# Kernel tuning notes

Hardware: AMD Instinct MI355X
Metric: run time of the kernel (lower is better)

## Reference

```python
import jax, jax.numpy as jnp
import numpy as np

N = 50000
E = 600000
H = 128   # hidden_channels (input to decoder)
O = 128   # output_channels (LSTM hidden size)
S = 8     # seq_len


def setup_inputs() -> dict:
    key = jax.random.key(0)
    ks = jax.random.split(key, 10)
    x = jax.random.normal(ks[0], (N, H), dtype=jnp.float32)
    c = jax.random.normal(ks[1], (N, H), dtype=jnp.float32)
    edge_index = jax.random.randint(ks[2], (2, E), 0, N, dtype=jnp.int64)
    # GCNConv weights (PyG: out = norm_agg(x @ W) + b)
    sc = lambda fan_in: 1.0 / np.sqrt(fan_in)
    Wh = jax.random.uniform(ks[3], (H, O), jnp.float32, -sc(H), sc(H))
    bh = jnp.zeros((O,), jnp.float32)
    Wc = jax.random.uniform(ks[4], (H, O), jnp.float32, -sc(H), sc(H))
    bc = jnp.zeros((O,), jnp.float32)
    # per-timestep cell convs: GCNConv(H + O, 4*O)
    Wcell = jax.random.uniform(ks[5], (S, H + O, 4 * O), jnp.float32, -sc(H + O), sc(H + O))
    bcell = jnp.zeros((S, 4 * O), jnp.float32)
    return {"x": x, "c": c, "edge_index": edge_index,
            "Wh": Wh, "bh": bh, "Wc": Wc, "bc": bc,
            "Wcell": Wcell, "bcell": bcell}


def _gcn(feat, W, b, src, dst, dinv):
    # PyG GCNConv with default add_self_loops=True, edge_weight=None:
    # out = D^{-1/2}(A+I)D^{-1/2} (feat @ W) + b
    xw = feat @ W                                   # [N, C_out]
    norm = (dinv[src] * dinv[dst])[:, None]         # [E, 1]
    agg = jax.ops.segment_sum(xw[src] * norm, dst, num_segments=N)
    agg = agg + (dinv * dinv)[:, None] * xw         # self-loop term
    return agg + b


def reference(x, c, edge_index, Wh, bh, Wc, bc, Wcell, bcell):
    src = edge_index[0]
    dst = edge_index[1]
    # degree (with self-loops, unit edge weights); computed on target index
    deg = jax.ops.segment_sum(jnp.ones((E,), jnp.float32), dst, num_segments=N) + 1.0
    dinv = 1.0 / jnp.sqrt(deg)

    h_cur = _gcn(x, Wh, bh, src, dst, dinv)
    c_cur = _gcn(c, Wc, bc, src, dst, dinv)

    def step(carry, params):
        h, cs = carry
        W, b = params
        combined = jnp.concatenate([x, h], axis=1)          # [N, H+O]
        cc = _gcn(combined, W, b, src, dst, dinv)           # [N, 4O]
        cc_f, cc_i, cc_o, cc_g = jnp.split(cc, 4, axis=1)
        f = jax.nn.sigmoid(cc_f)
        i = jax.nn.sigmoid(cc_i)
        o = jax.nn.sigmoid(cc_o)
        g = jnp.tanh(cc_g)
        c_next = f * cs + i * g
        h_next = o * jnp.tanh(c_next)
        return (h_next, c_next), h_next

    (h_fin, c_fin), hs = jax.lax.scan(step, (h_cur, c_cur), (Wcell, bcell))
    return hs, (h_fin, c_fin)  # hs: [S, N, O]
```

## Files before the change

### kernel.cpp

```cpp
#include <hip/hip_runtime.h>
#include <hip/hip_bf16.h>
#include <hip/hip_fp16.h>
#include <cstddef>


#define TPB 256

typedef __attribute__((ext_vector_type(8))) short bf16x8;
typedef __attribute__((ext_vector_type(4))) float f32x4;

__device__ __forceinline__ float sigf(float x) {
    return 1.0f / (1.0f + __expf(-x));
}
__device__ __forceinline__ float tanhfast(float x) {
    return 1.0f - 2.0f / (__expf(2.0f * x) + 1.0f);
}


__global__ void k_hist(const int* __restrict__ dst, int* __restrict__ counts, int E) {
    int e = blockIdx.x * TPB + threadIdx.x;
    if (e < E) atomicAdd(&counts[dst[e]], 1);
}

__global__ void k_scan_block(const int* __restrict__ counts, int* __restrict__ offsets,
                             int* __restrict__ sums, int N) {
    __shared__ int s[TPB];
    int tid = threadIdx.x;
    int gid = blockIdx.x * TPB + tid;
    int v = (gid < N) ? counts[gid] : 0;
    s[tid] = v;
    __syncthreads();
    for (int d = 1; d < TPB; d <<= 1) {
        int t = (tid >= d) ? s[tid - d] : 0;
        __syncthreads();
        s[tid] += t;
        __syncthreads();
    }
    if (gid < N) offsets[gid] = s[tid] - v;
    if (tid == TPB - 1) sums[blockIdx.x] = s[tid];
}

__global__ void k_scan_tops(int* __restrict__ sums, int nb) {
    __shared__ int s[TPB];
    int tid = threadIdx.x;
    int v = (tid < nb) ? sums[tid] : 0;
    s[tid] = v;
    __syncthreads();
    for (int d = 1; d < TPB; d <<= 1) {
        int t = (tid >= d) ? s[tid - d] : 0;
        __syncthreads();
        s[tid] += t;
        __syncthreads();
    }
    if (tid < nb) sums[tid] = s[tid] - v;
}

__global__ void k_scan_finish(const int* __restrict__ counts, int* __restrict__ offsets,
                              const int* __restrict__ sums, int* __restrict__ cursor,
                              float* __restrict__ dinv, int N, int E) {
    int gid = blockIdx.x * TPB + threadIdx.x;
    if (gid < N) {
        int off = offsets[gid] + sums[blockIdx.x];
        offsets[gid] = off;
        cursor[gid]  = off;
        dinv[gid]    = rsqrtf((float)(counts[gid] + 1));
    }
    if (gid == 0) offsets[N] = E;
}

__global__ void k_csr_scatter(const int* __restrict__ src, const int* __restrict__ dst,
                              const float* __restrict__ dinv, int* __restrict__ cursor,
                              int* __restrict__ csr_src, float* __restrict__ csr_w, int E) {
    int e = blockIdx.x * TPB + threadIdx.x;
    if (e >= E) return;
    int d = dst[e], s = src[e];
    int pos = atomicAdd(&cursor[d], 1);
    csr_src[pos] = s;
    csr_w[pos] = dinv[s] * dinv[d];
}


__global__ void k_f32tof16(const float* __restrict__ in, __half* __restrict__ out, int n4) {
    int i = blockIdx.x * TPB + threadIdx.x;
    if (i >= n4) return;
    float4 v = ((const float4*)in)[i];
    __half2 lo = __floats2half2_rn(v.x, v.y);
    __half2 hi = __floats2half2_rn(v.z, v.w);
    ((__half2*)out)[2 * i]     = lo;
    ((__half2*)out)[2 * i + 1] = hi;
}


__global__ __launch_bounds__(TPB) void k_aggregate_h(
        const __half* __restrict__ feat, __hip_bfloat16* __restrict__ agg,
        const int* __restrict__ offsets, const int* __restrict__ csr_src,
        const float* __restrict__ csr_w, const float* __restrict__ dinv, int N) {
    int node = blockIdx.x * 4 + (threadIdx.x >> 6);
    if (node >= N) return;
    int lane = threadIdx.x & 63;
    const __half2* f2 = (const __half2*)feat;
    float2 self = __half22float2(f2[(size_t)node * 64 + lane]);
    float di = dinv[node];
    float w0 = di * di;
    float accx = w0 * self.x, accy = w0 * self.y;
    int b = offsets[node], e = offsets[node + 1];
    int k = b;
    for (; k + 1 < e; k += 2) {
        int s0 = csr_src[k], s1 = csr_src[k + 1];
        float wa = csr_w[k], wb = csr_w[k + 1];
        float2 v0 = __half22float2(f2[(size_t)s0 * 64 + lane]);
        float2 v1 = __half22float2(f2[(size_t)s1 * 64 + lane]);
        accx = fmaf(wa, v0.x, accx);
        accy = fmaf(wa, v0.y, accy);
        accx = fmaf(wb, v1.x, accx);
        accy = fmaf(wb, v1.y, accy);
    }
    if (k < e) {
        int s = csr_src[k];
        float w = csr_w[k];
        float2 v = __half22float2(f2[(size_t)s * 64 + lane]);
        accx = fmaf(w, v.x, accx);
        accy = fmaf(w, v.y, accy);
    }
    __hip_bfloat162 r;
    r.x = __float2bfloat16(accx);
    r.y = __float2bfloat16(accy);
    ((__hip_bfloat162*)agg)[(size_t)node * 64 + lane] = r;
}

__global__ __launch_bounds__(TPB) void k_aggregate_h2(
        const __half* __restrict__ fa, const __half* __restrict__ fb,
        __hip_bfloat16* __restrict__ aggA, __hip_bfloat16* __restrict__ aggB,
        const int* __restrict__ offsets, const int* __restrict__ csr_src,
        const float* __restrict__ csr_w, const float* __restrict__ dinv, int N) {
    int node = blockIdx.x * 4 + (threadIdx.x >> 6);
    if (node >= N) return;
    int lane = threadIdx.x & 63;
    const __half2* fa2 = (const __half2*)fa;
    const __half2* fb2 = (const __half2*)fb;
    size_t selfIdx = (size_t)node * 64 + lane;
    float di = dinv[node];
    float w0 = di * di;
    float2 sa = __half22float2(fa2[selfIdx]);
    float2 sb = __half22float2(fb2[selfIdx]);
    float ax = w0 * sa.x, ay = w0 * sa.y;
    float bx = w0 * sb.x, by = w0 * sb.y;
    int b = offsets[node], e = offsets[node + 1];
    for (int k = b; k < e; ++k) {
        int s = csr_src[k];
        float w = csr_w[k];
        size_t si = (size_t)s * 64 + lane;
        float2 va = __half22float2(fa2[si]);
        float2 vb = __half22float2(fb2[si]);
        ax = fmaf(w, va.x, ax);
        ay = fmaf(w, va.y, ay);
        bx = fmaf(w, vb.x, bx);
        by = fmaf(w, vb.y, by);
    }
    __hip_bfloat162 ra, rb;
    ra.x = __float2bfloat16(ax); ra.y = __float2bfloat16(ay);
    rb.x = __float2bfloat16(bx); rb.y = __float2bfloat16(by);
    ((__hip_bfloat162*)aggA)[selfIdx] = ra;
    ((__hip_bfloat162*)aggB)[selfIdx] = rb;
}


__global__ void k_pack_w128(const float* __restrict__ W, __hip_bfloat16* __restrict__ Wp) {
    int idx = blockIdx.x * TPB + threadIdx.x;
    if (idx >= 16384) return;
    int j = idx & 7, lane = (idx >> 3) & 63, pblk = (idx >> 9) & 7, ks = idx >> 12;
    int k = ks * 32 + (lane >> 4) * 8 + j;
    int col = pblk * 16 + (lane & 15);
    Wp[idx] = __float2bfloat16(W[k * 128 + col]);
}

__global__ void k_pack_wcell(const float* __restrict__ W, __hip_bfloat16* __restrict__ Wp, int S) {
    int idx = blockIdx.x * TPB + threadIdx.x;
    if (idx >= S * 131072) return;
    int j = idx & 7, lane = (idx >> 3) & 63, pblk = (idx >> 9) & 31;
    int ks = (idx >> 14) & 7, s = idx >> 17;
    int p = pblk * 16 + (lane & 15);
    int jcol = p >> 2, gate = p & 3;
    int k = ks * 32 + (lane >> 4) * 8 + j;
    Wp[idx] = __float2bfloat16(W[(size_t)s * 131072 + k * 512 + gate * 128 + jcol]);
}


__global__ __launch_bounds__(TPB) void k_gemm_t(
        const __hip_bfloat16* __restrict__ Ap,
        const __hip_bfloat16* __restrict__ featb,
        const float* __restrict__ bias, float* __restrict__ Cout,
        __half* __restrict__ outh, int N) {
    __shared__ __align__(16) short Bs[128 * 40];
    int tid = threadIdx.x;
    int wave = tid >> 6, lane = tid & 63;
    int w_p = wave >> 1, w_n = wave & 1;
    int n0 = blockIdx.x * 128;
    int quad = lane >> 4, m16 = lane & 15;
    f32x4 zero = {0.f, 0.f, 0.f, 0.f};
    f32x4 acc[4][4];
    #pragma unroll
    for (int t = 0; t < 4; ++t)
        #pragma unroll
        for (int g = 0; g < 4; ++g) acc[t][g] = zero;

    for (int ks = 0; ks < 4; ++ks) {
        int kbase = ks * 32;
        __syncthreads();
        #pragma unroll
        for (int it = 0; it < 2; ++it) {
            int lin = it * TPB + tid;
            int row = lin >> 2, seg = lin & 3;
            int node = n0 + row;
            f32x4 v = zero;
            if (node < N) v = *(const f32x4*)(featb + (size_t)node * 128 + kbase + seg * 8);
            *(f32x4*)&Bs[row * 40 + seg * 8] = v;
        }
        __syncthreads();
        bf16x8 a[4], b[4];
        #pragma unroll
        for (int t = 0; t < 4; ++t)
            a[t] = *(const bf16x8*)(Ap + (((size_t)ks * 8 + w_p * 4 + t) * 64 + lane) * 8);
        #pragma unroll
        for (int g = 0; g < 4; ++g)
            b[g] = *(const bf16x8*)&Bs[(w_n * 64 + g * 16 + m16) * 40 + quad * 8];
        #pragma unroll
        for (int t = 0; t < 4; ++t)
            #pragma unroll
            for (int g = 0; g < 4; ++g)
                acc[t][g] = __builtin_amdgcn_mfma_f32_16x16x32_bf16(a[t], b[g], acc[t][g], 0, 0, 0);
    }
    #pragma unroll
    for (int t = 0; t < 4; ++t) {
        int p = w_p * 64 + t * 16 + quad * 4;
        f32x4 bv = *(const f32x4*)(bias + p);
        #pragma unroll
        for (int g = 0; g < 4; ++g) {
            int nd = n0 + w_n * 64 + g * 16 + m16;
            if (nd < N) {
                f32x4 o = acc[t][g] + bv;
                if (Cout) *(f32x4*)(Cout + (size_t)nd * 128 + p) = o;
                if (outh) {
                    __half2 lo = __floats2half2_rn(o.x, o.y);
                    __half2 hi = __floats2half2_rn(o.z, o.w);
                    __half2* hp = (__half2*)(outh + (size_t)nd * 128 + p);
                    hp[0] = lo;
                    hp[1] = hi;
                }
            }
        }
    }
}


__global__ __launch_bounds__(TPB) void k_cell_t(
        const __hip_bfloat16* __restrict__ Ap,
        const __hip_bfloat16* __restrict__ axb, const __hip_bfloat16* __restrict__ ahb,
        const float* __restrict__ bias,
        float* __restrict__ cbuf, float* __restrict__ hout,
        __half* __restrict__ houth,
        float* __restrict__ hfin, int N) {
    __shared__ __align__(16) short Bs[128 * 40];
    int tid = threadIdx.x;
    int wave = tid >> 6, lane = tid & 63;
    int w_p = wave >> 1, w_n = wave & 1;
    int n0 = blockIdx.x * 128;
    int p0 = blockIdx.y * 128;
    int quad = lane >> 4, m16 = lane & 15;
    f32x4 zero = {0.f, 0.f, 0.f, 0.f};
    f32x4 acc[4][4];
    #pragma unroll
    for (int t = 0; t < 4; ++t)
        #pragma unroll
        for (int g = 0; g < 4; ++g) acc[t][g] = zero;

    for (int ks = 0; ks < 8; ++ks) {
        const __hip_bfloat16* fsrc = (ks < 4) ? axb : ahb;
        int kbase = (ks & 3) * 32;
        __syncthreads();
        #pragma unroll
        for (int it = 0; it < 2; ++it) {
            int lin = it * TPB + tid;
            int row = lin >> 2, seg = lin & 3;
            int node = n0 + row;
            f32x4 v = zero;
            if (node < N) v = *(const f32x4*)(fsrc + (size_t)node * 128 + kbase + seg * 8);
            *(f32x4*)&Bs[row * 40 + seg * 8] = v;
        }
        __syncthreads();
        bf16x8 a[4], b[4];
        #pragma unroll
        for (int t = 0; t < 4; ++t)
            a[t] = *(const bf16x8*)(Ap + (((size_t)ks * 32 + (p0 >> 4) + w_p * 4 + t) * 64 + lane) * 8);
        #pragma unroll
        for (int g = 0; g < 4; ++g)
            b[g] = *(const bf16x8*)&Bs[(w_n * 64 + g * 16 + m16) * 40 + quad * 8];
        #pragma unroll
        for (int t = 0; t < 4; ++t)
            #pragma unroll
            for (int g = 0; g < 4; ++g)
                acc[t][g] = __builtin_amdgcn_mfma_f32_16x16x32_bf16(a[t], b[g], acc[t][g], 0, 0, 0);
    }
    #pragma unroll
    for (int t = 0; t < 4; ++t) {
        int p = p0 + w_p * 64 + t * 16 + quad * 4;
        int jcol = p >> 2;
        float bf = bias[jcol], bi = bias[128 + jcol], bo = bias[256 + jcol], bg = bias[384 + jcol];
        #pragma unroll
        for (int g = 0; g < 4; ++g) {
            int nd = n0 + w_n * 64 + g * 16 + m16;
            if (nd < N) {
                float fv = sigf(acc[t][g].x + bf);
                float iv = sigf(acc[t][g].y + bi);
                float ov = sigf(acc[t][g].z + bo);
                float gv = tanhfast(acc[t][g].w + bg);
                size_t idx = (size_t)nd * 128 + jcol;
                float cp = cbuf[idx];
                float cn = fmaf(fv, cp, iv * gv);
                cbuf[idx] = cn;
                float hn = ov * tanhfast(cn);
                hout[idx] = hn;
                houth[idx] = __float2half(hn);
                if (hfin) hfin[idx] = hn;
            }
        }
    }
}


extern "C" void kernel_launch(void* const* d_in, const int* in_sizes, int n_in,
                              void* d_out, int out_size, void* d_ws, size_t ws_size,
                              hipStream_t stream) {
    const float* x  = (const float*)d_in[0];
    const float* c  = (const float*)d_in[1];
    const int*   ei = (const int*)d_in[2];
    const float* Wh = (const float*)d_in[3];
    const float* bh = (const float*)d_in[4];
    const float* Wc = (const float*)d_in[5];
    const float* bc = (const float*)d_in[6];
    const float* Wcell = (const float*)d_in[7];
    const float* bcell = (const float*)d_in[8];
    float* out = (float*)d_out;

    const int N = in_sizes[0] / 128;
    const int E = in_sizes[2] / 2;
    const int S = in_sizes[7] / (256 * 512);
    const int* srcp = ei;
    const int* dstp = ei + E;

    float* hs   = out;
    float* hfin = out + (size_t)S * N * 128;
    float* cbuf = hfin + (size_t)N * 128;

    char* w = (char*)d_ws;
    size_t off = 0;
    auto alloc = [&](size_t bytes) -> void* {
        void* p = w + off;
        off += (bytes + 255) & ~(size_t)255;
        return p;
    };
    int*   counts  = (int*)alloc((size_t)N * 4);
    int*   offsets = (int*)alloc((size_t)(N + 1) * 4);
    int*   cursor  = (int*)alloc((size_t)N * 4);
    int*   sums    = (int*)alloc(256 * 4);
    int*   csr_src = (int*)alloc((size_t)E * 4);
    float* csr_w   = (float*)alloc((size_t)E * 4);
    float* dinv    = (float*)alloc((size_t)N * 4);
    __hip_bfloat16* axb = (__hip_bfloat16*)alloc((size_t)N * 128 * 2);
    __hip_bfloat16* acb = (__hip_bfloat16*)alloc((size_t)N * 128 * 2);
    __half* xh = (__half*)alloc((size_t)N * 128 * 2);
    __half* ch = (__half*)alloc((size_t)N * 128 * 2);
    __half* hh = (__half*)alloc((size_t)N * 128 * 2);
    __hip_bfloat16* WhP = (__hip_bfloat16*)alloc(16384 * 2);
    __hip_bfloat16* WcP = (__hip_bfloat16*)alloc(16384 * 2);
    __hip_bfloat16* WcellP = (__hip_bfloat16*)alloc((size_t)S * 131072 * 2);
    (void)ws_size; (void)n_in; (void)out_size;

    hipMemsetAsync(counts, 0, (size_t)N * 4, stream);
    int eblk = (E + TPB - 1) / TPB;
    int nb   = (N + TPB - 1) / TPB;
    k_hist<<<eblk, TPB, 0, stream>>>(dstp, counts, E);
    k_scan_block<<<nb, TPB, 0, stream>>>(counts, offsets, sums, N);
    k_scan_tops<<<1, TPB, 0, stream>>>(sums, nb);
    k_scan_finish<<<nb, TPB, 0, stream>>>(counts, offsets, sums, cursor, dinv, N, E);
    k_csr_scatter<<<eblk, TPB, 0, stream>>>(srcp, dstp, dinv, cursor, csr_src, csr_w, E);

    k_pack_w128<<<64, TPB, 0, stream>>>(Wh, WhP);
    k_pack_w128<<<64, TPB, 0, stream>>>(Wc, WcP);
    k_pack_wcell<<<(S * 131072 + TPB - 1) / TPB, TPB, 0, stream>>>(Wcell, WcellP, S);

    int n4 = N * 128 / 4;
    int cb = (n4 + TPB - 1) / TPB;
    k_f32tof16<<<cb, TPB, 0, stream>>>(x, xh, n4);
    k_f32tof16<<<cb, TPB, 0, stream>>>(c, ch, n4);

    int nagg = (N + 3) / 4;
    int ngt  = (N + 127) / 128;
    k_aggregate_h2<<<nagg, TPB, 0, stream>>>(xh, ch, axb, acb, offsets, csr_src, csr_w, dinv, N);
    k_gemm_t<<<ngt, TPB, 0, stream>>>(WhP, axb, bh, nullptr, hh, N);
    k_gemm_t<<<ngt, TPB, 0, stream>>>(WcP, acb, bc, cbuf, nullptr, N);

    for (int s = 0; s < S; ++s) {
        k_aggregate_h<<<nagg, TPB, 0, stream>>>(hh, acb, offsets, csr_src, csr_w, dinv, N);
        k_cell_t<<<dim3(ngt, 4), TPB, 0, stream>>>(
            WcellP + (size_t)s * 131072, axb, acb, bcell + (size_t)s * 512,
            cbuf, hs + (size_t)s * N * 128, hh, (s == S - 1) ? hfin : nullptr, N);
    }
}
```

Before: 1.518 ms.

## Interleave CSR src/weight, unroll aggregation, and stage full node tile once in cell GEMM

The CSR source index and edge weight now sit together in one int2 array, so each edge needs a single 8-byte load instead of two separate loads. The aggregation loops are unrolled further to keep more gathers in flight. The cell kernel now stages the whole 128-node by 256-K feature tile in LDS once and loops over all four gate-column blocks inside one block. This removes the 4x re-read of features across blockIdx.y and the per-k-step barriers. In exchange it uses about 80KB of LDS per block and launches a quarter as many blocks, which lowers occupancy and parallelism.

```diff
diff --git a/kernel.cpp b/kernel.cpp
--- a/kernel.cpp
+++ b/kernel.cpp
@@ -70,13 +70,15 @@
 
 __global__ void k_csr_scatter(const int* __restrict__ src, const int* __restrict__ dst,
                               const float* __restrict__ dinv, int* __restrict__ cursor,
-                              int* __restrict__ csr_src, float* __restrict__ csr_w, int E) {
+                              int2* __restrict__ csr_sw, int E) {
     int e = blockIdx.x * TPB + threadIdx.x;
     if (e >= E) return;
     int d = dst[e], s = src[e];
     int pos = atomicAdd(&cursor[d], 1);
-    csr_src[pos] = s;
-    csr_w[pos] = dinv[s] * dinv[d];
+    int2 r;
+    r.x = s;
+    r.y = __float_as_int(dinv[s] * dinv[d]);
+    csr_sw[pos] = r;
 }
 
 
@@ -93,8 +95,8 @@
 
 __global__ __launch_bounds__(TPB) void k_aggregate_h(
         const __half* __restrict__ feat, __hip_bfloat16* __restrict__ agg,
-        const int* __restrict__ offsets, const int* __restrict__ csr_src,
-        const float* __restrict__ csr_w, const float* __restrict__ dinv, int N) {
+        const int* __restrict__ offsets, const int2* __restrict__ sw,
+        const float* __restrict__ dinv, int N) {
     int node = blockIdx.x * 4 + (threadIdx.x >> 6);
     if (node >= N) return;
     int lane = threadIdx.x & 63;
@@ -105,20 +107,23 @@
     float accx = w0 * self.x, accy = w0 * self.y;
     int b = offsets[node], e = offsets[node + 1];
     int k = b;
-    for (; k + 1 < e; k += 2) {
-        int s0 = csr_src[k], s1 = csr_src[k + 1];
-        float wa = csr_w[k], wb = csr_w[k + 1];
-        float2 v0 = __half22float2(f2[(size_t)s0 * 64 + lane]);
-        float2 v1 = __half22float2(f2[(size_t)s1 * 64 + lane]);
-        accx = fmaf(wa, v0.x, accx);
-        accy = fmaf(wa, v0.y, accy);
-        accx = fmaf(wb, v1.x, accx);
-        accy = fmaf(wb, v1.y, accy);
-    }
-    if (k < e) {
-        int s = csr_src[k];
-        float w = csr_w[k];
-        float2 v = __half22float2(f2[(size_t)s * 64 + lane]);
+    for (; k + 3 < e; k += 4) {
+        int2 e0 = sw[k], e1 = sw[k + 1], e2 = sw[k + 2], e3 = sw[k + 3];
+        float2 v0 = __half22float2(f2[(size_t)e0.x * 64 + lane]);
+        float2 v1 = __half22float2(f2[(size_t)e1.x * 64 + lane]);
+        float2 v2 = __half22float2(f2[(size_t)e2.x * 64 + lane]);
+        float2 v3 = __half22float2(f2[(size_t)e3.x * 64 + lane]);
+        float wa = __int_as_float(e0.y), wb = __int_as_float(e1.y);
+        float wc = __int_as_float(e2.y), wd = __int_as_float(e3.y);
+        accx = fmaf(wa, v0.x, accx); accy = fmaf(wa, v0.y, accy);
+        accx = fmaf(wb, v1.x, accx); accy = fmaf(wb, v1.y, accy);
+        accx = fmaf(wc, v2.x, accx); accy = fmaf(wc, v2.y, accy);
+        accx = fmaf(wd, v3.x, accx); accy = fmaf(wd, v3.y, accy);
+    }
+    for (; k < e; ++k) {
+        int2 e0 = sw[k];
+        float2 v = __half22float2(f2[(size_t)e0.x * 64 + lane]);
+        float w = __int_as_float(e0.y);
         accx = fmaf(w, v.x, accx);
         accy = fmaf(w, v.y, accy);
     }
@@ -131,8 +136,8 @@
 __global__ __launch_bounds__(TPB) void k_aggregate_h2(
         const __half* __restrict__ fa, const __half* __restrict__ fb,
         __hip_bfloat16* __restrict__ aggA, __hip_bfloat16* __restrict__ aggB,
-        const int* __restrict__ offsets, const int* __restrict__ csr_src,
-        const float* __restrict__ csr_w, const float* __restrict__ dinv, int N) {
+        const int* __restrict__ offsets, const int2* __restrict__ sw,
+        const float* __restrict__ dinv, int N) {
     int node = blockIdx.x * 4 + (threadIdx.x >> 6);
     if (node >= N) return;
     int lane = threadIdx.x & 63;
@@ -146,16 +151,29 @@
     float ax = w0 * sa.x, ay = w0 * sa.y;
     float bx = w0 * sb.x, by = w0 * sb.y;
     int b = offsets[node], e = offsets[node + 1];
-    for (int k = b; k < e; ++k) {
-        int s = csr_src[k];
-        float w = csr_w[k];
-        size_t si = (size_t)s * 64 + lane;
-        float2 va = __half22float2(fa2[si]);
-        float2 vb = __half22float2(fb2[si]);
-        ax = fmaf(w, va.x, ax);
-        ay = fmaf(w, va.y, ay);
-        bx = fmaf(w, vb.x, bx);
-        by = fmaf(w, vb.y, by);
+    int k = b;
+    for (; k + 1 < e; k += 2) {
+        int2 e0 = sw[k], e1 = sw[k + 1];
+        size_t i0 = (size_t)e0.x * 64 + lane;
+        size_t i1 = (size_t)e1.x * 64 + lane;
+        float2 va0 = __half22float2(fa2[i0]);
+        float2 vb0 = __half22float2(fb2[i0]);
+        float2 va1 = __half22float2(fa2[i1]);
+        float2 vb1 = __half22float2(fb2[i1]);
+        float wa = __int_as_float(e0.y), wb = __int_as_float(e1.y);
+        ax = fmaf(wa, va0.x, ax); ay = fmaf(wa, va0.y, ay);
+        bx = fmaf(wa, vb0.x, bx); by = fmaf(wa, vb0.y, by);
+        ax = fmaf(wb, va1.x, ax); ay = fmaf(wb, va1.y, ay);
+        bx = fmaf(wb, vb1.x, bx); by = fmaf(wb, vb1.y, by);
+    }
+    if (k < e) {
+        int2 e0 = sw[k];
+        size_t i0 = (size_t)e0.x * 64 + lane;
+        float2 va = __half22float2(fa2[i0]);
+        float2 vb = __half22float2(fb2[i0]);
+        float w = __int_as_float(e0.y);
+        ax = fmaf(w, va.x, ax); ay = fmaf(w, va.y, ay);
+        bx = fmaf(w, vb.x, bx); by = fmaf(w, vb.y, by);
     }
     __hip_bfloat162 ra, rb;
     ra.x = __float2bfloat16(ax); ra.y = __float2bfloat16(ay);
@@ -260,68 +278,72 @@
         float* __restrict__ cbuf, float* __restrict__ hout,
         __half* __restrict__ houth,
         float* __restrict__ hfin, int N) {
-    __shared__ __align__(16) short Bs[128 * 40];
+    __shared__ __align__(16) short Bs[8][128 * 40];
     int tid = threadIdx.x;
     int wave = tid >> 6, lane = tid & 63;
     int w_p = wave >> 1, w_n = wave & 1;
     int n0 = blockIdx.x * 128;
-    int p0 = blockIdx.y * 128;
     int quad = lane >> 4, m16 = lane & 15;
     f32x4 zero = {0.f, 0.f, 0.f, 0.f};
-    f32x4 acc[4][4];
+
     #pragma unroll
-    for (int t = 0; t < 4; ++t)
-        #pragma unroll
-        for (int g = 0; g < 4; ++g) acc[t][g] = zero;
-
-    for (int ks = 0; ks < 8; ++ks) {
+    for (int it = 0; it < 16; ++it) {
+        int ks = it >> 1;
+        int lin = ((it & 1) << 8) + tid;
+        int row = lin >> 2, seg = lin & 3;
         const __hip_bfloat16* fsrc = (ks < 4) ? axb : ahb;
-        int kbase = (ks & 3) * 32;
-        __syncthreads();
-        #pragma unroll
-        for (int it = 0; it < 2; ++it) {
-            int lin = it * TPB + tid;
-            int row = lin >> 2, seg = lin & 3;
-            int node = n0 + row;
-            f32x4 v = zero;
-            if (node < N) v = *(const f32x4*)(fsrc + (size_t)node * 128 + kbase + seg * 8);
-            *(f32x4*)&Bs[row * 40 + seg * 8] = v;
+        int node = n0 + row;
+        f32x4 v = zero;
+        if (node < N) v = *(const f32x4*)(fsrc + (size_t)node * 128 + (ks & 3) * 32 + seg * 8);
+        *(f32x4*)&Bs[ks][row * 40 + seg * 8] = v;
+    }
+    __syncthreads();
+
+    for (int p0i = 0; p0i < 4; ++p0i) {
+        f32x4 acc[4][4];
+        #pragma unroll
+        for (int t = 0; t < 4; ++t)
+            #pragma unroll
+            for (int g = 0; g < 4; ++g) acc[t][g] = zero;
+
+        #pragma unroll
+        for (int ks = 0; ks < 8; ++ks) {
+            bf16x8 a[4], b[4];
+            #pragma unroll
+            for (int t = 0; t < 4; ++t)
+                a[t] = *(const bf16x8*)(Ap + (((size_t)ks * 32 + p0i * 8 + w_p * 4 + t) * 64 + lane) * 8);
+            #pragma unroll
+            for (int g = 0; g < 4; ++g)
+                b[g] = *(const bf16x8*)&Bs[ks][(w_n * 64 + g * 16 + m16) * 40 + quad * 8];
+            #pragma unroll
+            for (int t = 0; t < 4; ++t)
+                #pragma unroll
+                for (int g = 0; g < 4; ++g)
+                    acc[t][g] = __builtin_amdgcn_mfma_f32_16x16x32_bf16(a[t], b[g], acc[t][g], 0, 0, 0);
         }
-        __syncthreads();
-        bf16x8 a[4], b[4];
-        #pragma unroll
-        for (int t = 0; t < 4; ++t)
-            a[t] = *(const bf16x8*)(Ap + (((size_t)ks * 32 + (p0 >> 4) + w_p * 4 + t) * 64 + lane) * 8);
-        #pragma unroll
-        for (int g = 0; g < 4; ++g)
-            b[g] = *(const bf16x8*)&Bs[(w_n * 64 + g * 16 + m16) * 40 + quad * 8];
-        #pragma unroll
-        for (int t = 0; t < 4; ++t)
-            #pragma unroll
-            for (int g = 0; g < 4; ++g)
-                acc[t][g] = __builtin_amdgcn_mfma_f32_16x16x32_bf16(a[t], b[g], acc[t][g], 0, 0, 0);
-    }
-    #pragma unroll
-    for (int t = 0; t < 4; ++t) {
-        int p = p0 + w_p * 64 + t * 16 + quad * 4;
-        int jcol = p >> 2;
-        float bf = bias[jcol], bi = bias[128 + jcol], bo = bias[256 + jcol], bg = bias[384 + jcol];
-        #pragma unroll
-        for (int g = 0; g < 4; ++g) {
-            int nd = n0 + w_n * 64 + g * 16 + m16;
-            if (nd < N) {
-                float fv = sigf(acc[t][g].x + bf);
-                float iv = sigf(acc[t][g].y + bi);
-                float ov = sigf(acc[t][g].z + bo);
-                float gv = tanhfast(acc[t][g].w + bg);
-                size_t idx = (size_t)nd * 128 + jcol;
-                float cp = cbuf[idx];
-                float cn = fmaf(fv, cp, iv * gv);
-                cbuf[idx] = cn;
-                float hn = ov * tanhfast(cn);
-                hout[idx] = hn;
-                houth[idx] = __float2half(hn);
-                if (hfin) hfin[idx] = hn;
+
+        #pragma unroll
+        for (int t = 0; t < 4; ++t) {
+            int p = p0i * 128 + w_p * 64 + t * 16 + quad * 4;
+            int jcol = p >> 2;
+            float bf = bias[jcol], bi = bias[128 + jcol], bo = bias[256 + jcol], bg = bias[384 + jcol];
+            #pragma unroll
+            for (int g = 0; g < 4; ++g) {
+                int nd = n0 + w_n * 64 + g * 16 + m16;
+                if (nd < N) {
+                    float fv = sigf(acc[t][g].x + bf);
+                    float iv = sigf(acc[t][g].y + bi);
+                    float ov = sigf(acc[t][g].z + bo);
+                    float gv = tanhfast(acc[t][g].w + bg);
+                    size_t idx = (size_t)nd * 128 + jcol;
+                    float cp = cbuf[idx];
+                    float cn = fmaf(fv, cp, iv * gv);
+                    cbuf[idx] = cn;
+                    float hn = ov * tanhfast(cn);
+                    hout[idx] = hn;
+                    houth[idx] = __float2half(hn);
+                    if (hfin) hfin[idx] = hn;
+                }
             }
         }
     }
@@ -363,8 +385,7 @@
     int*   offsets = (int*)alloc((size_t)(N + 1) * 4);
     int*   cursor  = (int*)alloc((size_t)N * 4);
     int*   sums    = (int*)alloc(256 * 4);
-    int*   csr_src = (int*)alloc((size_t)E * 4);
-    float* csr_w   = (float*)alloc((size_t)E * 4);
+    int2*  csr_sw  = (int2*)alloc((size_t)E * 8);
     float* dinv    = (float*)alloc((size_t)N * 4);
     __hip_bfloat16* axb = (__hip_bfloat16*)alloc((size_t)N * 128 * 2);
     __hip_bfloat16* acb = (__hip_bfloat16*)alloc((size_t)N * 128 * 2);
@@ -383,7 +404,7 @@
     k_scan_block<<<nb, TPB, 0, stream>>>(counts, offsets, sums, N);
     k_scan_tops<<<1, TPB, 0, stream>>>(sums, nb);
     k_scan_finish<<<nb, TPB, 0, stream>>>(counts, offsets, sums, cursor, dinv, N, E);
-    k_csr_scatter<<<eblk, TPB, 0, stream>>>(srcp, dstp, dinv, cursor, csr_src, csr_w, E);
+    k_csr_scatter<<<eblk, TPB, 0, stream>>>(srcp, dstp, dinv, cursor, csr_sw, E);
 
     k_pack_w128<<<64, TPB, 0, stream>>>(Wh, WhP);
     k_pack_w128<<<64, TPB, 0, stream>>>(Wc, WcP);
@@ -396,13 +417,13 @@
 
     int nagg = (N + 3) / 4;
     int ngt  = (N + 127) / 128;
-    k_aggregate_h2<<<nagg, TPB, 0, stream>>>(xh, ch, axb, acb, offsets, csr_src, csr_w, dinv, N);
+    k_aggregate_h2<<<nagg, TPB, 0, stream>>>(xh, ch, axb, acb, offsets, csr_sw, dinv, N);
     k_gemm_t<<<ngt, TPB, 0, stream>>>(WhP, axb, bh, nullptr, hh, N);
     k_gemm_t<<<ngt, TPB, 0, stream>>>(WcP, acb, bc, cbuf, nullptr, N);
 
     for (int s = 0; s < S; ++s) {
-        k_aggregate_h<<<nagg, TPB, 0, stream>>>(hh, acb, offsets, csr_src, csr_w, dinv, N);
-        k_cell_t<<<dim3(ngt, 4), TPB, 0, stream>>>(
+        k_aggregate_h<<<nagg, TPB, 0, stream>>>(hh, acb, offsets, csr_sw, dinv, N);
+        k_cell_t<<<ngt, TPB, 0, stream>>>(
             WcellP + (size_t)s * 131072, axb, acb, bcell + (size_t)s * 512,
             cbuf, hs + (size_t)s * N * 128, hh, (s == S - 1) ? hfin : nullptr, N);
     }
```

Result: faster. 1.346 ms (-11.3%).
